# Kernel optimization log

Measured on AMD Instinct MI355X. Metric: run time of the kernel, lower is better.

The kernel has to match this reference:

```python
import jax, jax.numpy as jnp
import numpy as np

RETURN_SHAPE = (128, 128)


def dht2(x):
    # Discrete Hartley Transform over the spatial axes (2, 3):
    # H = Re(FFT) - Im(FFT). Unnormalized, matching scipy.fft default.
    f = jnp.fft.fftn(x, axes=(2, 3))
    return f.real - f.imag


def setup_inputs() -> dict:
    key = jax.random.key(0)
    x = jax.random.normal(key, (8, 64, 256, 256), dtype=jnp.float32)
    return {"x": x}


def reference(x) -> jnp.ndarray:
    # Spectral pooling: DHT -> center crop in frequency domain -> DHT.
    h_out, w_out = RETURN_SHAPE
    H, W = x.shape[2], x.shape[3]
    d = dht2(x)
    sh = (H - h_out) // 2
    sw = (W - w_out) // 2
    cropped = d[:, :, sh:sh + h_out, sw:sw + w_out]
    return dht2(cropped).astype(jnp.float32)
```

## Files before the change

kernel.cpp:

```cpp
#include <hip/hip_runtime.h>
#include <math.h>


typedef __attribute__((ext_vector_type(8))) short bfrag;
typedef __attribute__((ext_vector_type(4))) float ffrag;

#define PI2_256 0.0245436926061702597f
#define PI2_128 0.0490873852123405194f

__device__ __forceinline__ unsigned short f2bf(float f) {
    union { float f; unsigned int u; } v; v.f = f;
    unsigned int r = v.u + 0x7fffu + ((v.u >> 16) & 1u);
    return (unsigned short)(r >> 16);
}

__device__ __forceinline__ bfrag pack8(float4 a, float4 b) {
    bfrag r;
    r[0] = (short)f2bf(a.x); r[1] = (short)f2bf(a.y);
    r[2] = (short)f2bf(a.z); r[3] = (short)f2bf(a.w);
    r[4] = (short)f2bf(b.x); r[5] = (short)f2bf(b.y);
    r[6] = (short)f2bf(b.z); r[7] = (short)f2bf(b.w);
    return r;
}

__device__ __forceinline__ uint2 packlohi(ffrag a) {
    uint2 r;
    r.x = (unsigned int)f2bf(a[0]) | ((unsigned int)f2bf(a[1]) << 16);
    r.y = (unsigned int)f2bf(a[2]) | ((unsigned int)f2bf(a[3]) << 16);
    return r;
}

template<int NCOLS, int K, int NTH>
__device__ __forceinline__ void stageB(const unsigned short* __restrict__ src,
                                       unsigned short* __restrict__ Lb, int t)
{
    constexpr int CHUNKS = NCOLS * K / 8;
#pragma unroll
    for (int i = 0; i < CHUNKS / NTH; ++i) {
        const int o = (t + i * NTH) * 8;
        const int j = o / K;
        const int k = o - j * K;
        const uint4 v = *(const uint4*)(src + o);
        *(uint4*)&Lb[j * K + (((k >> 3) ^ (j & 7)) << 3)] = v;
    }
}

template<int K>
__device__ __forceinline__ bfrag ldsB(const unsigned short* __restrict__ Lb, int j, int k)
{
    return *(const bfrag*)&Lb[j * K + (((k >> 3) ^ (j & 7)) << 3)];
}

__global__ __launch_bounds__(256) void gen_tables(unsigned short* __restrict__ ws)
{
    const int id = blockIdx.x * 256 + threadIdx.x;
    {
        const int j = id >> 8, m = id & 255;
        const int mult = (j < 128) ? (64 + j) : (320 - j);
        const int idx = (mult * m) & 255;
        float s, c; sincosf((float)idx * PI2_256, &s, &c);
        ws[id] = f2bf(c + s);
    }
    {
        const int u = id >> 9, k = id & 511;
        const int up = 64 + u;
        float s, c, val;
        if (k < 256) { sincosf((float)((up * k) & 255) * PI2_256, &s, &c); val = c; }
        else         { sincosf((float)((up * (k - 256)) & 255) * PI2_256, &s, &c); val = s; }
        ws[65536 + id] = f2bf(val);
    }
    if (id < 32768) {
        {
            const int j = id >> 7, m = id & 127;
            const int mult = (j < 128) ? j : (256 - j);
            const int idx = (mult * m) & 127;
            float s, c; sincosf((float)idx * PI2_128, &s, &c);
            ws[131072 + id] = f2bf(c + s);
        }
        {
            const int u = id >> 8, k = id & 255;
            float s, c, val;
            if (k < 128) { sincosf((float)((u * k) & 127) * PI2_128, &s, &c); val = c; }
            else         { sincosf((float)((u * (k - 128)) & 127) * PI2_128, &s, &c); val = s; }
            ws[163840 + id] = f2bf(val);
        }
    }
}

__global__ __launch_bounds__(256, 2) void pass1(const float* __restrict__ X,
                                                const unsigned short* __restrict__ ws,
                                                unsigned short* __restrict__ Ct)
{
    __shared__ unsigned short Lb[64 * 256];

    const int t  = threadIdx.x;
    const int w  = t >> 6;
    const int ln = t & 15;
    const int q  = (t & 63) >> 4;
    const int img = blockIdx.x >> 2;
    const int h   = blockIdx.x & 3;

    stageB<64, 256, 256>(ws + h * 16384, Lb, t);
    __syncthreads();

    const float* __restrict__ Xi = X + (size_t)img * 65536;

    ffrag acc[4][4];
#pragma unroll
    for (int mt = 0; mt < 4; ++mt)
#pragma unroll
        for (int nt = 0; nt < 4; ++nt)
            acc[mt][nt] = (ffrag){0.f, 0.f, 0.f, 0.f};

#pragma unroll
    for (int kk = 0; kk < 8; ++kk) {
        const int k = kk * 32 + q * 8;
        bfrag A[4];
#pragma unroll
        for (int mt = 0; mt < 4; ++mt) {
            const float* xp = Xi + (size_t)(64 * w + 16 * mt + ln) * 256 + k;
            const float4 x0 = *(const float4*)xp;
            const float4 x1 = *(const float4*)(xp + 4);
            A[mt] = pack8(x0, x1);
        }
#pragma unroll
        for (int nt = 0; nt < 4; ++nt) {
            const bfrag B = ldsB<256>(Lb, nt * 16 + ln, k);
#pragma unroll
            for (int mt = 0; mt < 4; ++mt)
                acc[mt][nt] = __builtin_amdgcn_mfma_f32_16x16x32_bf16(A[mt], B, acc[mt][nt], 0, 0, 0);
        }
    }

    __syncthreads();
#pragma unroll
    for (int mt = 0; mt < 4; ++mt) {
#pragma unroll
        for (int nt = 0; nt < 4; ++nt) {
            const int cl = nt * 16 + ln;
            const int n2 = 16 * w + 4 * mt + q;
            const int phys = cl * 256 + (((n2 ^ ((cl & 7) << 3)) << 2));
            *(uint2*)&Lb[phys] = packlohi(acc[mt][nt]);
        }
    }
    __syncthreads();
    unsigned short* __restrict__ Co = Ct + (size_t)img * 65536 + 16384 * h;
#pragma unroll
    for (int j = 0; j < 8; ++j) {
        const int o   = (t + j * 256) * 8;
        const int row = o >> 8;
        const int ch  = (o & 255) >> 2;
        const int phys = row * 256 + (((ch ^ ((row & 7) << 3)) << 2));
        *(uint4*)&Co[o] = *(const uint4*)&Lb[phys];
    }
}

__global__ __launch_bounds__(256, 2) void pass2(const unsigned short* __restrict__ Ct,
                                                const unsigned short* __restrict__ ws,
                                                unsigned short* __restrict__ Dc)
{
    __shared__ unsigned short Lb[64 * 512];

    const int t  = threadIdx.x;
    const int w  = t >> 6;
    const int ln = t & 15;
    const int q  = (t & 63) >> 4;
    const int img = blockIdx.x >> 1;
    const int hu  = blockIdx.x & 1;

    stageB<64, 512, 256>(ws + 65536 + hu * 32768, Lb, t);
    __syncthreads();

    const unsigned short* __restrict__ Abase = Ct + (size_t)img * 65536;

    ffrag acc[2][4];
#pragma unroll
    for (int mt = 0; mt < 2; ++mt)
#pragma unroll
        for (int nt = 0; nt < 4; ++nt)
            acc[mt][nt] = (ffrag){0.f, 0.f, 0.f, 0.f};

#pragma unroll
    for (int kh = 0; kh < 2; ++kh) {
#pragma unroll
        for (int kk = 0; kk < 8; ++kk) {
            const int k = kk * 32 + q * 8;
            const int kfull = kh * 256 + k;
            bfrag A[2];
#pragma unroll
            for (int mt = 0; mt < 2; ++mt) {
                const int v = 32 * w + 16 * mt + ln;
                A[mt] = *(const bfrag*)(Abase + (size_t)(v + kh * 128) * 256 + k);
            }
#pragma unroll
            for (int nt = 0; nt < 4; ++nt) {
                const bfrag B = ldsB<512>(Lb, nt * 16 + ln, kfull);
#pragma unroll
                for (int mt = 0; mt < 2; ++mt)
                    acc[mt][nt] = __builtin_amdgcn_mfma_f32_16x16x32_bf16(A[mt], B, acc[mt][nt], 0, 0, 0);
            }
        }
    }
#pragma unroll
    for (int mt = 0; mt < 2; ++mt) {
        unsigned short* __restrict__ Do = Dc + (size_t)img * 16384 + 32 * w + 16 * mt + 4 * q;
#pragma unroll
        for (int nt = 0; nt < 4; ++nt) {
            *(uint2*)&Do[(size_t)(64 * hu + nt * 16 + ln) * 128] = packlohi(acc[mt][nt]);
        }
    }
}

__global__ __launch_bounds__(256, 2) void stage2f(const unsigned short* __restrict__ Dc,
                                                  const unsigned short* __restrict__ ws,
                                                  float* __restrict__ out)
{
    __shared__ unsigned short Dcb[128 * 128];
    __shared__ unsigned short PQ2[64 * 256];

    const int t  = threadIdx.x;
    const int w  = t >> 6;
    const int ln = t & 15;
    const int q  = (t & 63) >> 4;
    const int img = blockIdx.x;

    float* __restrict__ G = out + (size_t)img * 16384;
    const unsigned short* __restrict__ W3 = ws + 131072;
    const unsigned short* __restrict__ W4 = ws + 163840;

    {
        const unsigned short* __restrict__ src = Dc + (size_t)img * 16384;
#pragma unroll
        for (int j = 0; j < 8; ++j) {
            const int o  = (t + j * 256) * 8;
            const int p  = o >> 7;
            const int m0 = o & 127;
            const int gran = (m0 >> 3) ^ (p & 7);
            *(uint4*)&Dcb[p * 128 + gran * 8] = *(const uint4*)(src + o);
        }
    }
    __syncthreads();

    for (int vh = 0; vh < 2; ++vh) {
        ffrag acc[2][8];
#pragma unroll
        for (int mt = 0; mt < 2; ++mt)
#pragma unroll
            for (int nt = 0; nt < 8; ++nt)
                acc[mt][nt] = (ffrag){0.f, 0.f, 0.f, 0.f};

        const int p0 = 32 * w;
        for (int kk = 0; kk < 4; ++kk) {
            const int k = kk * 32 + q * 8;
            bfrag A[2];
#pragma unroll
            for (int mt = 0; mt < 2; ++mt) {
                const int p = p0 + 16 * mt + ln;
                const int g = (k >> 3) ^ (p & 7);
                A[mt] = *(const bfrag*)&Dcb[p * 128 + g * 8];
            }
#pragma unroll
            for (int nt = 0; nt < 8; ++nt) {
                const int c = nt * 16 + ln;
                const int j = (c < 64) ? (64 * vh + c) : (128 + 64 * vh + (c - 64));
                const bfrag B = *(const bfrag*)(W3 + j * 128 + k);
#pragma unroll
                for (int mt = 0; mt < 2; ++mt)
                    acc[mt][nt] = __builtin_amdgcn_mfma_f32_16x16x32_bf16(A[mt], B, acc[mt][nt], 0, 0, 0);
            }
        }
        __syncthreads();
#pragma unroll
        for (int mt = 0; mt < 2; ++mt) {
#pragma unroll
            for (int nt = 0; nt < 8; ++nt) {
                const int c  = nt * 16 + ln;
                const int v  = c & 63;
                const int kb = ((c < 64) ? 0 : 128) + p0 + 16 * mt + 4 * q;
                const uint2 lohi = packlohi(acc[mt][nt]);
                const int phys = v * 256 + (((kb >> 3) ^ (v & 7)) << 3) + (kb & 7);
                *(uint2*)&PQ2[phys] = lohi;
            }
        }
        __syncthreads();

        ffrag o2[2][4];
#pragma unroll
        for (int mt = 0; mt < 2; ++mt)
#pragma unroll
            for (int nt = 0; nt < 4; ++nt)
                o2[mt][nt] = (ffrag){0.f, 0.f, 0.f, 0.f};

        const int u0 = 32 * w;
        for (int kk = 0; kk < 8; ++kk) {
            const int k = kk * 32 + q * 8;
            bfrag A[2];
#pragma unroll
            for (int mt = 0; mt < 2; ++mt)
                A[mt] = *(const bfrag*)(W4 + (size_t)(u0 + 16 * mt + ln) * 256 + k);
#pragma unroll
            for (int nt = 0; nt < 4; ++nt) {
                const int v = nt * 16 + ln;
                const int g = (k >> 3) ^ (v & 7);
                const bfrag B = *(const bfrag*)&PQ2[v * 256 + (g << 3)];
#pragma unroll
                for (int mt = 0; mt < 2; ++mt)
                    o2[mt][nt] = __builtin_amdgcn_mfma_f32_16x16x32_bf16(A[mt], B, o2[mt][nt], 0, 0, 0);
            }
        }
#pragma unroll
        for (int mt = 0; mt < 2; ++mt) {
#pragma unroll
            for (int nt = 0; nt < 4; ++nt) {
#pragma unroll
                for (int r = 0; r < 4; ++r) {
                    const int u = u0 + 16 * mt + 4 * q + r;
                    const int v = 64 * vh + nt * 16 + ln;
                    G[u * 128 + v] = o2[mt][nt][r];
                }
            }
        }
    }
}

__global__ __launch_bounds__(512, 2) void stage1_old(const float* __restrict__ X,
                                                     const unsigned short* __restrict__ ws,
                                                     float* __restrict__ dc)
{
    __shared__ unsigned short PQt[128 * 512];

    const int t  = threadIdx.x;
    const int w  = t >> 6;
    const int ln = t & 15;
    const int q  = (t & 63) >> 4;
    const int img = blockIdx.x;

    const float* __restrict__ Xi = X + (size_t)img * 65536;
    const unsigned short* __restrict__ W1 = ws;
    const unsigned short* __restrict__ W2 = ws + 65536;

    {
        ffrag acc[2][16];
#pragma unroll
        for (int mt = 0; mt < 2; ++mt)
#pragma unroll
            for (int nt = 0; nt < 16; ++nt)
                acc[mt][nt] = (ffrag){0.f, 0.f, 0.f, 0.f};

        const int rowA0 = 32 * w;
        for (int kk = 0; kk < 8; ++kk) {
            const int k = kk * 32 + q * 8;
            bfrag A[2];
#pragma unroll
            for (int mt = 0; mt < 2; ++mt) {
                const float* xp = Xi + (size_t)(rowA0 + 16 * mt + ln) * 256 + k;
                const float4 x0 = *(const float4*)xp;
                const float4 x1 = *(const float4*)(xp + 4);
                A[mt] = pack8(x0, x1);
            }
#pragma unroll
            for (int nt = 0; nt < 16; ++nt) {
                const int j = nt * 16 + ln;
                const bfrag B = *(const bfrag*)(W1 + j * 256 + k);
#pragma unroll
                for (int mt = 0; mt < 2; ++mt)
                    acc[mt][nt] = __builtin_amdgcn_mfma_f32_16x16x32_bf16(A[mt], B, acc[mt][nt], 0, 0, 0);
            }
        }
#pragma unroll
        for (int mt = 0; mt < 2; ++mt) {
#pragma unroll
            for (int nt = 0; nt < 16; ++nt) {
                const int c  = nt * 16 + ln;
                const int v  = c & 127;
                const int kb = ((c < 128) ? 0 : 256) + rowA0 + 16 * mt + 4 * q;
                const uint2 lohi = packlohi(acc[mt][nt]);
                const int phys = v * 512 + (((kb >> 3) ^ (v & 7)) << 3) + (kb & 7);
                *(uint2*)&PQt[phys] = lohi;
            }
        }
    }
    __syncthreads();

    {
        ffrag acc[8];
#pragma unroll
        for (int nt = 0; nt < 8; ++nt) acc[nt] = (ffrag){0.f, 0.f, 0.f, 0.f};

        const int u0 = 16 * w;
        for (int kk = 0; kk < 16; ++kk) {
            const int k = kk * 32 + q * 8;
            const bfrag A = *(const bfrag*)(W2 + (size_t)(u0 + ln) * 512 + k);
#pragma unroll
            for (int nt = 0; nt < 8; ++nt) {
                const int v = nt * 16 + ln;
                const int g = (k >> 3) ^ (v & 7);
                const bfrag B = *(const bfrag*)&PQt[v * 512 + (g << 3)];
                acc[nt] = __builtin_amdgcn_mfma_f32_16x16x32_bf16(A, B, acc[nt], 0, 0, 0);
            }
        }
        float* __restrict__ D = dc + (size_t)img * 16384;
#pragma unroll
        for (int nt = 0; nt < 8; ++nt) {
#pragma unroll
            for (int r = 0; r < 4; ++r) {
                const int u = u0 + 4 * q + r;
                const int v = nt * 16 + ln;
                D[u * 128 + v] = acc[nt][r];
            }
        }
    }
}

__global__ __launch_bounds__(256, 2) void stage2_old(const unsigned short* __restrict__ ws,
                                                     float* __restrict__ io)
{
    __shared__ unsigned short Dcb[128 * 128];
    __shared__ unsigned short PQ2[64 * 256];

    const int t  = threadIdx.x;
    const int w  = t >> 6;
    const int ln = t & 15;
    const int q  = (t & 63) >> 4;
    const int img = blockIdx.x;

    float* __restrict__ G = io + (size_t)img * 16384;
    const unsigned short* __restrict__ W3 = ws + 131072;
    const unsigned short* __restrict__ W4 = ws + 163840;

    {
        const int p = t >> 1, half = t & 1;
        const float* src = G + p * 128 + half * 64;
#pragma unroll
        for (int g = 0; g < 8; ++g) {
            const float4 a = *(const float4*)(src + g * 8);
            const float4 b = *(const float4*)(src + g * 8 + 4);
            const int m0 = half * 64 + g * 8;
            const int gran = (m0 >> 3) ^ (p & 7);
            uint4 val;
            val.x = (unsigned int)f2bf(a.x) | ((unsigned int)f2bf(a.y) << 16);
            val.y = (unsigned int)f2bf(a.z) | ((unsigned int)f2bf(a.w) << 16);
            val.z = (unsigned int)f2bf(b.x) | ((unsigned int)f2bf(b.y) << 16);
            val.w = (unsigned int)f2bf(b.z) | ((unsigned int)f2bf(b.w) << 16);
            *(uint4*)&Dcb[p * 128 + gran * 8] = val;
        }
    }
    __syncthreads();

    for (int vh = 0; vh < 2; ++vh) {
        ffrag acc[2][8];
#pragma unroll
        for (int mt = 0; mt < 2; ++mt)
#pragma unroll
            for (int nt = 0; nt < 8; ++nt)
                acc[mt][nt] = (ffrag){0.f, 0.f, 0.f, 0.f};

        const int p0 = 32 * w;
        for (int kk = 0; kk < 4; ++kk) {
            const int k = kk * 32 + q * 8;
            bfrag A[2];
#pragma unroll
            for (int mt = 0; mt < 2; ++mt) {
                const int p = p0 + 16 * mt + ln;
                const int g = (k >> 3) ^ (p & 7);
                A[mt] = *(const bfrag*)&Dcb[p * 128 + g * 8];
            }
#pragma unroll
            for (int nt = 0; nt < 8; ++nt) {
                const int c = nt * 16 + ln;
                const int j = (c < 64) ? (64 * vh + c) : (128 + 64 * vh + (c - 64));
                const bfrag B = *(const bfrag*)(W3 + j * 128 + k);
#pragma unroll
                for (int mt = 0; mt < 2; ++mt)
                    acc[mt][nt] = __builtin_amdgcn_mfma_f32_16x16x32_bf16(A[mt], B, acc[mt][nt], 0, 0, 0);
            }
        }
        __syncthreads();
#pragma unroll
        for (int mt = 0; mt < 2; ++mt) {
#pragma unroll
            for (int nt = 0; nt < 8; ++nt) {
                const int c  = nt * 16 + ln;
                const int v  = c & 63;
                const int kb = ((c < 64) ? 0 : 128) + p0 + 16 * mt + 4 * q;
                const uint2 lohi = packlohi(acc[mt][nt]);
                const int phys = v * 256 + (((kb >> 3) ^ (v & 7)) << 3) + (kb & 7);
                *(uint2*)&PQ2[phys] = lohi;
            }
        }
        __syncthreads();

        ffrag o[2][4];
#pragma unroll
        for (int mt = 0; mt < 2; ++mt)
#pragma unroll
            for (int nt = 0; nt < 4; ++nt)
                o[mt][nt] = (ffrag){0.f, 0.f, 0.f, 0.f};

        const int u0 = 32 * w;
        for (int kk = 0; kk < 8; ++kk) {
            const int k = kk * 32 + q * 8;
            bfrag A[2];
#pragma unroll
            for (int mt = 0; mt < 2; ++mt)
                A[mt] = *(const bfrag*)(W4 + (size_t)(u0 + 16 * mt + ln) * 256 + k);
#pragma unroll
            for (int nt = 0; nt < 4; ++nt) {
                const int v = nt * 16 + ln;
                const int g = (k >> 3) ^ (v & 7);
                const bfrag B = *(const bfrag*)&PQ2[v * 256 + (g << 3)];
#pragma unroll
                for (int mt = 0; mt < 2; ++mt)
                    o[mt][nt] = __builtin_amdgcn_mfma_f32_16x16x32_bf16(A[mt], B, o[mt][nt], 0, 0, 0);
            }
        }
#pragma unroll
        for (int mt = 0; mt < 2; ++mt) {
#pragma unroll
            for (int nt = 0; nt < 4; ++nt) {
#pragma unroll
                for (int r = 0; r < 4; ++r) {
                    const int u = u0 + 16 * mt + 4 * q + r;
                    const int v = 64 * vh + nt * 16 + ln;
                    G[u * 128 + v] = o[mt][nt][r];
                }
            }
        }
    }
}

extern "C" void kernel_launch(void* const* d_in, const int* in_sizes, int n_in,
                              void* d_out, int out_size, void* d_ws, size_t ws_size,
                              hipStream_t stream)
{
    const float* x = (const float*)d_in[0];
    float* out = (float*)d_out;
    unsigned short* tw = (unsigned short*)d_ws;

    gen_tables<<<dim3(256), dim3(256), 0, stream>>>(tw);

    int G = 512;
    while (G > 1 && (size_t)163840 * (size_t)G + 393216 > ws_size) G >>= 1;

    if ((size_t)163840 * (size_t)G + 393216 <= ws_size) {
        unsigned short* regA = tw + 196608;
        unsigned short* regB = regA + (size_t)G * 65536;
        const int nchunks = 512 / G;
        for (int ci = 0; ci < nchunks; ++ci) {
            const float* xc = x + (size_t)ci * G * 65536;
            float* oc = out + (size_t)ci * G * 16384;
            pass1<<<dim3(4 * G), dim3(256), 0, stream>>>(xc, tw, regA);
            pass2<<<dim3(2 * G), dim3(256), 0, stream>>>(regA, tw, regB);
            stage2f<<<dim3(G), dim3(256), 0, stream>>>(regB, tw, oc);
        }
    } else {
        stage1_old<<<dim3(512), dim3(512), 0, stream>>>(x, tw, out);
        stage2_old<<<dim3(512), dim3(256), 0, stream>>>(tw, out);
    }
}
```

Before: 291.6 us.

## Remap blocks to XCD-local images and split final pass into two halves

Adds an XCD-aware block-to-image mapping so that all blocks working on one image land on the same XCD (block index mod 8), keeping intermediate data in that XCD's L2 across passes. The final stage is also split so each block handles one output half (vh), doubling the grid and removing the in-block loop over halves. The split makes each block redo the Dc staging load and share the twiddle reads, in exchange for more parallelism and shorter blocks.

```diff
diff --git a/kernel.cpp b/kernel.cpp
--- a/kernel.cpp
+++ b/kernel.cpp
@@ -30,6 +30,20 @@
     return r;
 }
 
+__device__ __forceinline__ void imgmap(int b, int nimgx, int bpi_log2,
+                                       int& img, int& sub)
+{
+    if (nimgx) {
+        const int xcd = b & 7;
+        const int s   = b >> 3;
+        img = xcd * nimgx + (s >> bpi_log2);
+        sub = s & ((1 << bpi_log2) - 1);
+    } else {
+        img = b >> bpi_log2;
+        sub = b & ((1 << bpi_log2) - 1);
+    }
+}
+
 template<int NCOLS, int K, int NTH>
 __device__ __forceinline__ void stageB(const unsigned short* __restrict__ src,
                                        unsigned short* __restrict__ Lb, int t)
@@ -89,7 +103,8 @@
 
 __global__ __launch_bounds__(256, 2) void pass1(const float* __restrict__ X,
                                                 const unsigned short* __restrict__ ws,
-                                                unsigned short* __restrict__ Ct)
+                                                unsigned short* __restrict__ Ct,
+                                                int nimgx)
 {
     __shared__ unsigned short Lb[64 * 256];
 
@@ -97,8 +112,8 @@
     const int w  = t >> 6;
     const int ln = t & 15;
     const int q  = (t & 63) >> 4;
-    const int img = blockIdx.x >> 2;
-    const int h   = blockIdx.x & 3;
+    int img, h;
+    imgmap(blockIdx.x, nimgx, 2, img, h);
 
     stageB<64, 256, 256>(ws + h * 16384, Lb, t);
     __syncthreads();
@@ -157,7 +172,8 @@
 
 __global__ __launch_bounds__(256, 2) void pass2(const unsigned short* __restrict__ Ct,
                                                 const unsigned short* __restrict__ ws,
-                                                unsigned short* __restrict__ Dc)
+                                                unsigned short* __restrict__ Dc,
+                                                int nimgx)
 {
     __shared__ unsigned short Lb[64 * 512];
 
@@ -165,8 +181,8 @@
     const int w  = t >> 6;
     const int ln = t & 15;
     const int q  = (t & 63) >> 4;
-    const int img = blockIdx.x >> 1;
-    const int hu  = blockIdx.x & 1;
+    int img, hu;
+    imgmap(blockIdx.x, nimgx, 1, img, hu);
 
     stageB<64, 512, 256>(ws + 65536 + hu * 32768, Lb, t);
     __syncthreads();
@@ -211,9 +227,10 @@
     }
 }
 
-__global__ __launch_bounds__(256, 2) void stage2f(const unsigned short* __restrict__ Dc,
-                                                  const unsigned short* __restrict__ ws,
-                                                  float* __restrict__ out)
+__global__ __launch_bounds__(256, 2) void pass34(const unsigned short* __restrict__ Dc,
+                                                 const unsigned short* __restrict__ ws,
+                                                 float* __restrict__ out,
+                                                 int nimgx)
 {
     __shared__ unsigned short Dcb[128 * 128];
     __shared__ unsigned short PQ2[64 * 256];
@@ -222,7 +239,8 @@
     const int w  = t >> 6;
     const int ln = t & 15;
     const int q  = (t & 63) >> 4;
-    const int img = blockIdx.x;
+    int img, vh;
+    imgmap(blockIdx.x, nimgx, 1, img, vh);
 
     float* __restrict__ G = out + (size_t)img * 16384;
     const unsigned short* __restrict__ W3 = ws + 131072;
@@ -241,83 +259,80 @@
     }
     __syncthreads();
 
-    for (int vh = 0; vh < 2; ++vh) {
-        ffrag acc[2][8];
+    ffrag acc[2][8];
+#pragma unroll
+    for (int mt = 0; mt < 2; ++mt)
+#pragma unroll
+        for (int nt = 0; nt < 8; ++nt)
+            acc[mt][nt] = (ffrag){0.f, 0.f, 0.f, 0.f};
+
+    const int p0 = 32 * w;
+    for (int kk = 0; kk < 4; ++kk) {
+        const int k = kk * 32 + q * 8;
+        bfrag A[2];
+#pragma unroll
+        for (int mt = 0; mt < 2; ++mt) {
+            const int p = p0 + 16 * mt + ln;
+            const int g = (k >> 3) ^ (p & 7);
+            A[mt] = *(const bfrag*)&Dcb[p * 128 + g * 8];
+        }
+#pragma unroll
+        for (int nt = 0; nt < 8; ++nt) {
+            const int c = nt * 16 + ln;
+            const int j = (c < 64) ? (64 * vh + c) : (128 + 64 * vh + (c - 64));
+            const bfrag B = *(const bfrag*)(W3 + j * 128 + k);
+#pragma unroll
+            for (int mt = 0; mt < 2; ++mt)
+                acc[mt][nt] = __builtin_amdgcn_mfma_f32_16x16x32_bf16(A[mt], B, acc[mt][nt], 0, 0, 0);
+        }
+    }
+#pragma unroll
+    for (int mt = 0; mt < 2; ++mt) {
+#pragma unroll
+        for (int nt = 0; nt < 8; ++nt) {
+            const int c  = nt * 16 + ln;
+            const int v  = c & 63;
+            const int kb = ((c < 64) ? 0 : 128) + p0 + 16 * mt + 4 * q;
+            const uint2 lohi = packlohi(acc[mt][nt]);
+            const int phys = v * 256 + (((kb >> 3) ^ (v & 7)) << 3) + (kb & 7);
+            *(uint2*)&PQ2[phys] = lohi;
+        }
+    }
+    __syncthreads();
+
+    ffrag o2[2][4];
+#pragma unroll
+    for (int mt = 0; mt < 2; ++mt)
+#pragma unroll
+        for (int nt = 0; nt < 4; ++nt)
+            o2[mt][nt] = (ffrag){0.f, 0.f, 0.f, 0.f};
+
+    const int u0 = 32 * w;
+    for (int kk = 0; kk < 8; ++kk) {
+        const int k = kk * 32 + q * 8;
+        bfrag A[2];
 #pragma unroll
         for (int mt = 0; mt < 2; ++mt)
-#pragma unroll
-            for (int nt = 0; nt < 8; ++nt)
-                acc[mt][nt] = (ffrag){0.f, 0.f, 0.f, 0.f};
-
-        const int p0 = 32 * w;
-        for (int kk = 0; kk < 4; ++kk) {
-            const int k = kk * 32 + q * 8;
-            bfrag A[2];
-#pragma unroll
-            for (int mt = 0; mt < 2; ++mt) {
-                const int p = p0 + 16 * mt + ln;
-                const int g = (k >> 3) ^ (p & 7);
-                A[mt] = *(const bfrag*)&Dcb[p * 128 + g * 8];
-            }
-#pragma unroll
-            for (int nt = 0; nt < 8; ++nt) {
-                const int c = nt * 16 + ln;
-                const int j = (c < 64) ? (64 * vh + c) : (128 + 64 * vh + (c - 64));
-                const bfrag B = *(const bfrag*)(W3 + j * 128 + k);
-#pragma unroll
-                for (int mt = 0; mt < 2; ++mt)
-                    acc[mt][nt] = __builtin_amdgcn_mfma_f32_16x16x32_bf16(A[mt], B, acc[mt][nt], 0, 0, 0);
-            }
-        }
-        __syncthreads();
-#pragma unroll
-        for (int mt = 0; mt < 2; ++mt) {
-#pragma unroll
-            for (int nt = 0; nt < 8; ++nt) {
-                const int c  = nt * 16 + ln;
-                const int v  = c & 63;
-                const int kb = ((c < 64) ? 0 : 128) + p0 + 16 * mt + 4 * q;
-                const uint2 lohi = packlohi(acc[mt][nt]);
-                const int phys = v * 256 + (((kb >> 3) ^ (v & 7)) << 3) + (kb & 7);
-                *(uint2*)&PQ2[phys] = lohi;
-            }
-        }
-        __syncthreads();
-
-        ffrag o2[2][4];
-#pragma unroll
-        for (int mt = 0; mt < 2; ++mt)
-#pragma unroll
-            for (int nt = 0; nt < 4; ++nt)
-                o2[mt][nt] = (ffrag){0.f, 0.f, 0.f, 0.f};
-
-        const int u0 = 32 * w;
-        for (int kk = 0; kk < 8; ++kk) {
-            const int k = kk * 32 + q * 8;
-            bfrag A[2];
+            A[mt] = *(const bfrag*)(W4 + (size_t)(u0 + 16 * mt + ln) * 256 + k);
+#pragma unroll
+        for (int nt = 0; nt < 4; ++nt) {
+            const int v = nt * 16 + ln;
+            const int g = (k >> 3) ^ (v & 7);
+            const bfrag B = *(const bfrag*)&PQ2[v * 256 + (g << 3)];
 #pragma unroll
             for (int mt = 0; mt < 2; ++mt)
-                A[mt] = *(const bfrag*)(W4 + (size_t)(u0 + 16 * mt + ln) * 256 + k);
-#pragma unroll
-            for (int nt = 0; nt < 4; ++nt) {
-                const int v = nt * 16 + ln;
-                const int g = (k >> 3) ^ (v & 7);
-                const bfrag B = *(const bfrag*)&PQ2[v * 256 + (g << 3)];
-#pragma unroll
-                for (int mt = 0; mt < 2; ++mt)
-                    o2[mt][nt] = __builtin_amdgcn_mfma_f32_16x16x32_bf16(A[mt], B, o2[mt][nt], 0, 0, 0);
-            }
-        }
-#pragma unroll
-        for (int mt = 0; mt < 2; ++mt) {
-#pragma unroll
-            for (int nt = 0; nt < 4; ++nt) {
-#pragma unroll
-                for (int r = 0; r < 4; ++r) {
-                    const int u = u0 + 16 * mt + 4 * q + r;
-                    const int v = 64 * vh + nt * 16 + ln;
-                    G[u * 128 + v] = o2[mt][nt][r];
-                }
+                o2[mt][nt] = __builtin_amdgcn_mfma_f32_16x16x32_bf16(A[mt], B, o2[mt][nt], 0, 0, 0);
+        }
+    }
+#pragma unroll
+    for (int mt = 0; mt < 2; ++mt) {
+#pragma unroll
+        for (int nt = 0; nt < 4; ++nt) {
+#pragma unroll
+            for (int r = 0; r < 4; ++r) {
+                const int u = u0 + 16 * mt + 4 * q + r;
+                const int v = 64 * vh + nt * 16 + ln;
+                G[u * 128 + v] = o2[mt][nt][r];
             }
         }
     }
@@ -545,13 +560,14 @@
     if ((size_t)163840 * (size_t)G + 393216 <= ws_size) {
         unsigned short* regA = tw + 196608;
         unsigned short* regB = regA + (size_t)G * 65536;
+        const int nimgx = ((G & 7) == 0) ? (G >> 3) : 0;
         const int nchunks = 512 / G;
         for (int ci = 0; ci < nchunks; ++ci) {
             const float* xc = x + (size_t)ci * G * 65536;
             float* oc = out + (size_t)ci * G * 16384;
-            pass1<<<dim3(4 * G), dim3(256), 0, stream>>>(xc, tw, regA);
-            pass2<<<dim3(2 * G), dim3(256), 0, stream>>>(regA, tw, regB);
-            stage2f<<<dim3(G), dim3(256), 0, stream>>>(regB, tw, oc);
+            pass1<<<dim3(4 * G), dim3(256), 0, stream>>>(xc, tw, regA, nimgx);
+            pass2<<<dim3(2 * G), dim3(256), 0, stream>>>(regA, tw, regB, nimgx);
+            pass34<<<dim3(2 * G), dim3(256), 0, stream>>>(regB, tw, oc, nimgx);
         }
     } else {
         stage1_old<<<dim3(512), dim3(512), 0, stream>>>(x, tw, out);
```

Result: no change. 289.2 us (-0.8%).
